# Kernel tuning notes

Hardware: AMD Instinct MI355X
Metric: run time of the kernel (lower is better)

The kernel has to match this reference:

```python
import jax, jax.numpy as jnp
import numpy as np

B, T = 128, 2048
O, E, L = 128, 512, 34  # o_size, embed_dim, num_letter


def setup_inputs() -> dict:
    key = jax.random.key(0)
    ks = jax.random.split(key, 16)
    u = lambda k, shape, s: jax.random.uniform(k, shape, jnp.float32, -s, s)
    hk = jax.random.normal(ks[0], (B, T, O), jnp.float32)
    hv = jax.random.normal(ks[1], (B, T, O), jnp.float32)
    y_1 = jax.random.normal(ks[2], (B, E), jnp.float32)
    c_1 = jax.random.normal(ks[3], (B, O), jnp.float32)
    sh_1 = jax.random.normal(ks[4], (B, O), jnp.float32)
    sc_1 = jax.random.normal(ks[5], (B, O), jnp.float32)
    # valid-length mask (each row has at least T//2 valid positions)
    lengths = jax.random.randint(ks[6], (B,), T // 2, T + 1)
    mask = (jnp.arange(T)[None, :] < lengths[:, None]).astype(jnp.float32)
    s_rnn = 1.0 / np.sqrt(O)
    W_ih = u(ks[7], (4 * O, O + E), s_rnn)
    b_ih = u(ks[8], (4 * O,), s_rnn)
    W_hh = u(ks[9], (4 * O, O), s_rnn)
    b_hh = u(ks[10], (4 * O,), s_rnn)
    s1 = 1.0 / np.sqrt(O)
    W1 = u(ks[11], (L, O), s1); b1 = u(ks[12], (L,), s1)
    W2 = u(ks[13], (L, O), s1); b2 = u(ks[14], (L,), s1)
    s3 = 1.0 / np.sqrt(L)
    W3 = u(ks[15], (L, L), s3); b3 = u(jax.random.fold_in(key, 99), (L,), s3)
    return {"hk": hk, "hv": hv, "y_1": y_1, "c_1": c_1, "sh_1": sh_1,
            "sc_1": sc_1, "mask": mask, "W_ih": W_ih, "b_ih": b_ih,
            "W_hh": W_hh, "b_hh": b_hh, "W1": W1, "b1": b1,
            "W2": W2, "b2": b2, "W3": W3, "b3": b3}


def reference(hk, hv, y_1, c_1, sh_1, sc_1, mask,
              W_ih, b_ih, W_hh, b_hh, W1, b1, W2, b2, W3, b3):
    # LSTMCell (PyTorch gate order: i, f, g, o)
    x = jnp.concatenate([y_1, c_1], axis=1)            # [B, O+E]
    gates = x @ W_ih.T + b_ih + sh_1 @ W_hh.T + b_hh   # [B, 4O]
    i, f, g, o = jnp.split(gates, 4, axis=1)
    sc = jax.nn.sigmoid(f) * sc_1 + jax.nn.sigmoid(i) * jnp.tanh(g)
    sh = jax.nn.sigmoid(o) * jnp.tanh(sc)
    # attention scores keyed on cell state sc (faithful to source)
    scores = jnp.einsum('bto,bo->bt', hk, sc)          # [B, T]
    attn = jax.nn.softmax(scores, axis=1) * mask
    attn = attn / jnp.sum(attn, axis=1, keepdims=True)
    c = jnp.einsum('bt,bto->bo', attn, hv)             # [B, O]
    out = jax.nn.relu(sh @ W1.T + b1 + c @ W2.T + b2)
    out = jax.nn.softmax(out @ W3.T + b3, axis=1)      # [B, L]
    return (out, c, sh, sc)
```

## Files before the change

kernel.cpp:

```cpp
#include <hip/hip_runtime.h>
#include <math.h>

#define BB 128
#define TT 2048
#define OO 128
#define EE 512
#define LL 34
#define XDIM 640
#define CHUNKS 16
#define CHUNK_LEN 128

__device__ __forceinline__ float sigmoidf_(float x) { return 1.0f / (1.0f + __expf(-x)); }

__global__ __launch_bounds__(256) void lstm_kernel(
    const float* __restrict__ y1, const float* __restrict__ c1,
    const float* __restrict__ sh1, const float* __restrict__ sc1,
    const float* __restrict__ Wih, const float* __restrict__ bih,
    const float* __restrict__ Whh, const float* __restrict__ bhh,
    float* __restrict__ out_sh, float* __restrict__ out_sc)
{
    __shared__ float xs[4][768];
    __shared__ float gbuf[4][4][16];
    const int tid = threadIdx.x;
    const int otile = blockIdx.x;
    const int qb = blockIdx.y * 4;

    for (int idx = tid; idx < 4 * 768; idx += 256) {
        int bi = idx / 768, k = idx - bi * 768;
        int b = qb + bi;
        float v;
        if (k < 512)      v = y1[b * EE + k];
        else if (k < 640) v = c1[b * OO + (k - 512)];
        else              v = sh1[b * OO + (k - 640)];
        xs[bi][k] = v;
    }
    __syncthreads();

    const int g = tid >> 6, l = tid & 63;
    #pragma unroll 2
    for (int i = 0; i < 16; ++i) {
        const int row = g * 128 + otile * 16 + i;
        const float* wr = Wih + (size_t)row * XDIM;
        float a0 = 0.f, a1 = 0.f, a2 = 0.f, a3 = 0.f;
        #pragma unroll
        for (int j = 0; j < 10; ++j) {
            float wv = wr[l + 64 * j];
            a0 += wv * xs[0][l + 64 * j];
            a1 += wv * xs[1][l + 64 * j];
            a2 += wv * xs[2][l + 64 * j];
            a3 += wv * xs[3][l + 64 * j];
        }
        const float* wh = Whh + (size_t)row * OO;
        #pragma unroll
        for (int j = 0; j < 2; ++j) {
            float wv = wh[l + 64 * j];
            a0 += wv * xs[0][640 + l + 64 * j];
            a1 += wv * xs[1][640 + l + 64 * j];
            a2 += wv * xs[2][640 + l + 64 * j];
            a3 += wv * xs[3][640 + l + 64 * j];
        }
        #pragma unroll
        for (int off = 32; off >= 1; off >>= 1) {
            a0 += __shfl_xor(a0, off);
            a1 += __shfl_xor(a1, off);
            a2 += __shfl_xor(a2, off);
            a3 += __shfl_xor(a3, off);
        }
        if (l == 0) {
            float bb = bih[row] + bhh[row];
            gbuf[g][0][i] = a0 + bb;
            gbuf[g][1][i] = a1 + bb;
            gbuf[g][2][i] = a2 + bb;
            gbuf[g][3][i] = a3 + bb;
        }
    }
    __syncthreads();

    if (tid < 64) {
        const int bi = tid >> 4, ol = tid & 15;
        const int b = qb + bi, o = otile * 16 + ol;
        float gi = gbuf[0][bi][ol], gf = gbuf[1][bi][ol];
        float gg = gbuf[2][bi][ol], go = gbuf[3][bi][ol];
        float sc = sigmoidf_(gf) * sc1[b * OO + o] + sigmoidf_(gi) * tanhf(gg);
        float sh = sigmoidf_(go) * tanhf(sc);
        out_sc[b * OO + o] = sc;
        out_sh[b * OO + o] = sh;
    }
}

__global__ __launch_bounds__(256) void scores_kernel(
    const float* __restrict__ hk, const float* __restrict__ mask,
    const float* __restrict__ sc, float* __restrict__ wbuf)
{
    const int b = blockIdx.y, chunk = blockIdx.x;
    const int tid = threadIdx.x;
    const int sg = tid >> 4, l = tid & 15;

    const float4 scA = *(const float4*)(sc + b * OO + l * 8);
    const float4 scB = *(const float4*)(sc + b * OO + l * 8 + 4);

    const int r0 = chunk * CHUNK_LEN + sg * 8;
    const float* mrow = mask + (size_t)b * TT + r0;
    const float* krow = hk + ((size_t)b * TT + r0) * OO;

    float s[8];
    #pragma unroll
    for (int i = 0; i < 8; ++i) {
        const bool valid = (mrow[i] != 0.f);
        float4 a = make_float4(0.f, 0.f, 0.f, 0.f);
        float4 c2 = make_float4(0.f, 0.f, 0.f, 0.f);
        if (valid) {
            a  = *(const float4*)(krow + (size_t)i * OO + l * 8);
            c2 = *(const float4*)(krow + (size_t)i * OO + l * 8 + 4);
        }
        s[i] = a.x * scA.x + a.y * scA.y + a.z * scA.z + a.w * scA.w
             + c2.x * scB.x + c2.y * scB.y + c2.z * scB.z + c2.w * scB.w;
    }
    #pragma unroll
    for (int i = 0; i < 8; ++i) {
        s[i] += __shfl_xor(s[i], 8);
        s[i] += __shfl_xor(s[i], 4);
        s[i] += __shfl_xor(s[i], 2);
        s[i] += __shfl_xor(s[i], 1);
    }
    float* wrow = wbuf + (size_t)b * TT + r0;
    #pragma unroll
    for (int i = 0; i < 8; ++i)
        if (l == i) wrow[i] = s[i];
}

__global__ __launch_bounds__(256) void softmax_kernel(
    float* __restrict__ wbuf, const float* __restrict__ mask)
{
    const int b = blockIdx.x, tid = threadIdx.x;
    const int lane = tid & 63, wv = tid >> 6;
    float* srow = wbuf + (size_t)b * TT;
    const float* mrow = mask + (size_t)b * TT;

    float sarr[8], earr[8];
    bool varr[8];
    float lm = -INFINITY;
    #pragma unroll
    for (int j = 0; j < 8; ++j) {
        int t = tid + 256 * j;
        sarr[j] = srow[t];
        varr[j] = (mrow[t] != 0.f);
        if (varr[j]) lm = fmaxf(lm, sarr[j]);
    }
    #pragma unroll
    for (int off = 32; off >= 1; off >>= 1) lm = fmaxf(lm, __shfl_xor(lm, off));
    __shared__ float red[4];
    if (lane == 0) red[wv] = lm;
    __syncthreads();
    const float M = fmaxf(fmaxf(red[0], red[1]), fmaxf(red[2], red[3]));

    float ls = 0.f;
    #pragma unroll
    for (int j = 0; j < 8; ++j) {
        earr[j] = varr[j] ? __expf(sarr[j] - M) : 0.f;
        ls += earr[j];
    }
    #pragma unroll
    for (int off = 32; off >= 1; off >>= 1) ls += __shfl_xor(ls, off);
    __syncthreads();
    if (lane == 0) red[wv] = ls;
    __syncthreads();
    const float inv = 1.f / (red[0] + red[1] + red[2] + red[3]);
    #pragma unroll
    for (int j = 0; j < 8; ++j) srow[tid + 256 * j] = earr[j] * inv;
}

__global__ __launch_bounds__(256) void wsum_kernel(
    const float* __restrict__ hv, const float* __restrict__ wbuf,
    float* __restrict__ ws_c)
{
    const int b = blockIdx.y, chunk = blockIdx.x;
    const int tid = threadIdx.x;
    __shared__ float wsh[CHUNK_LEN];
    __shared__ float pacc[8][128];

    if (tid < CHUNK_LEN)
        wsh[tid] = wbuf[(size_t)b * TT + chunk * CHUNK_LEN + tid];
    __syncthreads();

    const int o4 = tid & 31, rr = tid >> 5;
    const float* vbase = hv + ((size_t)b * TT + chunk * CHUNK_LEN) * OO + o4 * 4;
    float4 acc = make_float4(0.f, 0.f, 0.f, 0.f);
    #pragma unroll 8
    for (int j = 0; j < 16; ++j) {
        const int r = rr + 8 * j;
        const float wr = wsh[r];
        if (wr != 0.f) {
            float4 v = *(const float4*)(vbase + (size_t)r * OO);
            acc.x += wr * v.x;
            acc.y += wr * v.y;
            acc.z += wr * v.z;
            acc.w += wr * v.w;
        }
    }
    *(float4*)&pacc[rr][o4 * 4] = acc;
    __syncthreads();

    if (tid < 128) {
        float s = 0.f;
        #pragma unroll
        for (int i = 0; i < 8; ++i) s += pacc[i][tid];
        ws_c[((size_t)b * CHUNKS + chunk) * OO + tid] = s;
    }
}

__global__ __launch_bounds__(256) void final_kernel(
    const float* __restrict__ ws_c, const float* __restrict__ sh_in,
    const float* __restrict__ W1, const float* __restrict__ b1,
    const float* __restrict__ W2, const float* __restrict__ b2,
    const float* __restrict__ W3, const float* __restrict__ b3,
    float* __restrict__ out_p, float* __restrict__ out_c)
{
    const int b = blockIdx.x, tid = threadIdx.x;
    __shared__ float cbuf[128], shbuf[128], h1[LL], zz[LL], red2[2];

    if (tid < 128) {
        float s = 0.f;
        const float* base = ws_c + (size_t)b * CHUNKS * OO + tid;
        #pragma unroll
        for (int i = 0; i < CHUNKS; ++i) s += base[i * OO];
        cbuf[tid] = s;
        out_c[b * OO + tid] = s;
        shbuf[tid] = sh_in[b * OO + tid];
    }
    __syncthreads();

    const int o = tid >> 2, l2 = tid & 3;
    if (o < LL) {
        float a = 0.f;
        const float* w1r = W1 + o * OO;
        const float* w2r = W2 + o * OO;
        #pragma unroll 8
        for (int j = 0; j < 32; ++j) {
            int k = l2 + 4 * j;
            a += w1r[k] * shbuf[k] + w2r[k] * cbuf[k];
        }
        a += __shfl_xor(a, 1);
        a += __shfl_xor(a, 2);
        if (l2 == 0) h1[o] = fmaxf(a + b1[o] + b2[o], 0.f);
    }
    __syncthreads();

    if (o < LL) {
        float z = 0.f;
        const float* w3r = W3 + o * LL;
        for (int j = 0; j < 9; ++j) {
            int k = l2 + 4 * j;
            if (k < LL) z += w3r[k] * h1[k];
        }
        z += __shfl_xor(z, 1);
        z += __shfl_xor(z, 2);
        if (l2 == 0) zz[o] = z + b3[o];
    }
    __syncthreads();
    if (tid == 0) {
        float mm = zz[0];
        for (int i = 1; i < LL; i++) mm = fmaxf(mm, zz[i]);
        float ss = 0.f;
        for (int i = 0; i < LL; i++) ss += __expf(zz[i] - mm);
        red2[0] = mm; red2[1] = ss;
    }
    __syncthreads();
    if (tid < LL) out_p[b * LL + tid] = __expf(zz[tid] - red2[0]) / red2[1];
}

extern "C" void kernel_launch(void* const* d_in, const int* in_sizes, int n_in,
                              void* d_out, int out_size, void* d_ws, size_t ws_size,
                              hipStream_t stream) {
    (void)in_sizes; (void)n_in; (void)out_size; (void)ws_size;
    const float* hk   = (const float*)d_in[0];
    const float* hv   = (const float*)d_in[1];
    const float* y1   = (const float*)d_in[2];
    const float* c1   = (const float*)d_in[3];
    const float* sh1  = (const float*)d_in[4];
    const float* sc1  = (const float*)d_in[5];
    const float* mask = (const float*)d_in[6];
    const float* Wih  = (const float*)d_in[7];
    const float* bih  = (const float*)d_in[8];
    const float* Whh  = (const float*)d_in[9];
    const float* bhh  = (const float*)d_in[10];
    const float* W1   = (const float*)d_in[11];
    const float* b1   = (const float*)d_in[12];
    const float* W2   = (const float*)d_in[13];
    const float* b2   = (const float*)d_in[14];
    const float* W3   = (const float*)d_in[15];
    const float* b3   = (const float*)d_in[16];

    float* out    = (float*)d_out;
    float* out_c  = out + BB * LL;
    float* out_sh = out_c + BB * OO;
    float* out_sc = out_sh + BB * OO;

    float* wbuf = (float*)d_ws;
    float* ws_c = wbuf + (size_t)BB * TT;

    lstm_kernel<<<dim3(8, 32), 256, 0, stream>>>(y1, c1, sh1, sc1, Wih, bih, Whh, bhh,
                                                 out_sh, out_sc);
    scores_kernel<<<dim3(CHUNKS, BB), 256, 0, stream>>>(hk, mask, out_sc, wbuf);
    softmax_kernel<<<BB, 256, 0, stream>>>(wbuf, mask);
    wsum_kernel<<<dim3(CHUNKS, BB), 256, 0, stream>>>(hv, wbuf, ws_c);
    final_kernel<<<BB, 256, 0, stream>>>(ws_c, out_sh, W1, b1, W2, b2, W3, b3,
                                         out, out_c);
}
```

Before: 331.2 us.

## Fuse softmax into scores via per-chunk online max/sum, drop softmax kernel

Each scores block now computes a local max and exp-sum over its chunk, writes unnormalised exponentials plus a (max, sum) pair per chunk, and wsum rescales the chunk weights with the combined global max and sum. This removes the separate softmax kernel launch and its extra read/write pass over the score buffer. In exchange it adds a block-level reduction in scores and a small per-block combine in wsum, and it depends on the workspace being large enough to hold the new pbuf region.

```diff
diff --git a/kernel.cpp b/kernel.cpp
--- a/kernel.cpp
+++ b/kernel.cpp
@@ -90,7 +90,8 @@
 
 __global__ __launch_bounds__(256) void scores_kernel(
     const float* __restrict__ hk, const float* __restrict__ mask,
-    const float* __restrict__ sc, float* __restrict__ wbuf)
+    const float* __restrict__ sc, float* __restrict__ wbuf,
+    float2* __restrict__ pbuf)
 {
     const int b = blockIdx.y, chunk = blockIdx.x;
     const int tid = threadIdx.x;
@@ -104,12 +105,13 @@
     const float* krow = hk + ((size_t)b * TT + r0) * OO;
 
     float s[8];
+    bool val[8];
     #pragma unroll
     for (int i = 0; i < 8; ++i) {
-        const bool valid = (mrow[i] != 0.f);
+        val[i] = (mrow[i] != 0.f);
         float4 a = make_float4(0.f, 0.f, 0.f, 0.f);
         float4 c2 = make_float4(0.f, 0.f, 0.f, 0.f);
-        if (valid) {
+        if (val[i]) {
             a  = *(const float4*)(krow + (size_t)i * OO + l * 8);
             c2 = *(const float4*)(krow + (size_t)i * OO + l * 8 + 4);
         }
@@ -123,64 +125,64 @@
         s[i] += __shfl_xor(s[i], 2);
         s[i] += __shfl_xor(s[i], 1);
     }
+    float msg = -INFINITY;
+    #pragma unroll
+    for (int i = 0; i < 8; ++i) if (val[i]) msg = fmaxf(msg, s[i]);
+
+    __shared__ float sm[16], ssum[16];
+    if (l == 0) sm[sg] = msg;
+    __syncthreads();
+    float mc = sm[0];
+    #pragma unroll
+    for (int i = 1; i < 16; ++i) mc = fmaxf(mc, sm[i]);
+
+    float psum = 0.f;
+    float e[8];
+    #pragma unroll
+    for (int i = 0; i < 8; ++i) {
+        e[i] = val[i] ? __expf(s[i] - mc) : 0.f;
+        psum += e[i];
+    }
+    if (l == 0) ssum[sg] = psum;
     float* wrow = wbuf + (size_t)b * TT + r0;
     #pragma unroll
     for (int i = 0; i < 8; ++i)
-        if (l == i) wrow[i] = s[i];
-}
-
-__global__ __launch_bounds__(256) void softmax_kernel(
-    float* __restrict__ wbuf, const float* __restrict__ mask)
-{
-    const int b = blockIdx.x, tid = threadIdx.x;
-    const int lane = tid & 63, wv = tid >> 6;
-    float* srow = wbuf + (size_t)b * TT;
-    const float* mrow = mask + (size_t)b * TT;
-
-    float sarr[8], earr[8];
-    bool varr[8];
-    float lm = -INFINITY;
-    #pragma unroll
-    for (int j = 0; j < 8; ++j) {
-        int t = tid + 256 * j;
-        sarr[j] = srow[t];
-        varr[j] = (mrow[t] != 0.f);
-        if (varr[j]) lm = fmaxf(lm, sarr[j]);
-    }
-    #pragma unroll
-    for (int off = 32; off >= 1; off >>= 1) lm = fmaxf(lm, __shfl_xor(lm, off));
-    __shared__ float red[4];
-    if (lane == 0) red[wv] = lm;
-    __syncthreads();
-    const float M = fmaxf(fmaxf(red[0], red[1]), fmaxf(red[2], red[3]));
-
-    float ls = 0.f;
-    #pragma unroll
-    for (int j = 0; j < 8; ++j) {
-        earr[j] = varr[j] ? __expf(sarr[j] - M) : 0.f;
-        ls += earr[j];
-    }
-    #pragma unroll
-    for (int off = 32; off >= 1; off >>= 1) ls += __shfl_xor(ls, off);
-    __syncthreads();
-    if (lane == 0) red[wv] = ls;
-    __syncthreads();
-    const float inv = 1.f / (red[0] + red[1] + red[2] + red[3]);
-    #pragma unroll
-    for (int j = 0; j < 8; ++j) srow[tid + 256 * j] = earr[j] * inv;
+        if (l == i) wrow[i] = e[i];
+    __syncthreads();
+    if (tid == 0) {
+        float S = 0.f;
+        #pragma unroll
+        for (int i = 0; i < 16; ++i) S += ssum[i];
+        pbuf[(size_t)b * CHUNKS + chunk] = make_float2(mc, S);
+    }
 }
 
 __global__ __launch_bounds__(256) void wsum_kernel(
     const float* __restrict__ hv, const float* __restrict__ wbuf,
-    float* __restrict__ ws_c)
+    const float2* __restrict__ pbuf, float* __restrict__ ws_c)
 {
     const int b = blockIdx.y, chunk = blockIdx.x;
     const int tid = threadIdx.x;
+    __shared__ float marr[CHUNKS], Sarr[CHUNKS];
     __shared__ float wsh[CHUNK_LEN];
     __shared__ float pacc[8][128];
 
+    if (tid < CHUNKS) {
+        float2 p = pbuf[(size_t)b * CHUNKS + tid];
+        marr[tid] = p.x;
+        Sarr[tid] = p.y;
+    }
+    __syncthreads();
+    float M = marr[0];
+    #pragma unroll
+    for (int i = 1; i < CHUNKS; ++i) M = fmaxf(M, marr[i]);
+    float S = 0.f;
+    #pragma unroll
+    for (int i = 0; i < CHUNKS; ++i) S += Sarr[i] * __expf(marr[i] - M);
+    const float factor = __expf(marr[chunk] - M) / S;
+
     if (tid < CHUNK_LEN)
-        wsh[tid] = wbuf[(size_t)b * TT + chunk * CHUNK_LEN + tid];
+        wsh[tid] = wbuf[(size_t)b * TT + chunk * CHUNK_LEN + tid] * factor;
     __syncthreads();
 
     const int o4 = tid & 31, rr = tid >> 5;
@@ -296,14 +298,14 @@
     float* out_sh = out_c + BB * OO;
     float* out_sc = out_sh + BB * OO;
 
-    float* wbuf = (float*)d_ws;
-    float* ws_c = wbuf + (size_t)BB * TT;
+    float*  wbuf = (float*)d_ws;
+    float*  ws_c = wbuf + (size_t)BB * TT;
+    float2* pbuf = (float2*)(ws_c + (size_t)BB * CHUNKS * OO);
 
     lstm_kernel<<<dim3(8, 32), 256, 0, stream>>>(y1, c1, sh1, sc1, Wih, bih, Whh, bhh,
                                                  out_sh, out_sc);
-    scores_kernel<<<dim3(CHUNKS, BB), 256, 0, stream>>>(hk, mask, out_sc, wbuf);
-    softmax_kernel<<<BB, 256, 0, stream>>>(wbuf, mask);
-    wsum_kernel<<<dim3(CHUNKS, BB), 256, 0, stream>>>(hv, wbuf, ws_c);
+    scores_kernel<<<dim3(CHUNKS, BB), 256, 0, stream>>>(hk, mask, out_sc, wbuf, pbuf);
+    wsum_kernel<<<dim3(CHUNKS, BB), 256, 0, stream>>>(hv, wbuf, pbuf, ws_c);
     final_kernel<<<BB, 256, 0, stream>>>(ws_c, out_sh, W1, b1, W2, b2, W3, b3,
                                          out, out_c);
 }
```

Measured after the change: 328.2 us. About the same (-0.9%).

## Batch unconditional float4 loads in scores and weighted-sum kernels for memory parallelism

Applied to the files above, without the earlier changes.

Both streaming kernels are remapped so each half-wavefront reads a full 128-float row with contiguous float4 loads. Each thread issues eight independent loads before using any of them, which raises the number of memory requests in flight. The data-dependent skipping of masked or zero-weight rows is dropped, so every row of hk and hv is read. This trades extra bytes for regular, coalesced, branch-free loads. Correctness still relies on softmax applying the mask, and the cross-row reduction now uses an xor-32 shuffle plus a 4-way shared reduction.

```diff
diff --git a/kernel.cpp b/kernel.cpp
--- a/kernel.cpp
+++ b/kernel.cpp
@@ -89,44 +89,37 @@
 }
 
 __global__ __launch_bounds__(256) void scores_kernel(
-    const float* __restrict__ hk, const float* __restrict__ mask,
-    const float* __restrict__ sc, float* __restrict__ wbuf)
+    const float* __restrict__ hk, const float* __restrict__ sc,
+    float* __restrict__ wbuf)
 {
     const int b = blockIdx.y, chunk = blockIdx.x;
     const int tid = threadIdx.x;
-    const int sg = tid >> 4, l = tid & 15;
-
-    const float4 scA = *(const float4*)(sc + b * OO + l * 8);
-    const float4 scB = *(const float4*)(sc + b * OO + l * 8 + 4);
-
-    const int r0 = chunk * CHUNK_LEN + sg * 8;
-    const float* mrow = mask + (size_t)b * TT + r0;
-    const float* krow = hk + ((size_t)b * TT + r0) * OO;
-
-    float s[8];
-    #pragma unroll
-    for (int i = 0; i < 8; ++i) {
-        const bool valid = (mrow[i] != 0.f);
-        float4 a = make_float4(0.f, 0.f, 0.f, 0.f);
-        float4 c2 = make_float4(0.f, 0.f, 0.f, 0.f);
-        if (valid) {
-            a  = *(const float4*)(krow + (size_t)i * OO + l * 8);
-            c2 = *(const float4*)(krow + (size_t)i * OO + l * 8 + 4);
-        }
-        s[i] = a.x * scA.x + a.y * scA.y + a.z * scA.z + a.w * scA.w
-             + c2.x * scB.x + c2.y * scB.y + c2.z * scB.z + c2.w * scB.w;
-    }
-    #pragma unroll
-    for (int i = 0; i < 8; ++i) {
-        s[i] += __shfl_xor(s[i], 8);
-        s[i] += __shfl_xor(s[i], 4);
-        s[i] += __shfl_xor(s[i], 2);
-        s[i] += __shfl_xor(s[i], 1);
-    }
-    float* wrow = wbuf + (size_t)b * TT + r0;
-    #pragma unroll
-    for (int i = 0; i < 8; ++i)
-        if (l == i) wrow[i] = s[i];
+    const int w = tid >> 6, lane = tid & 63;
+    const int h = lane >> 5, l5 = lane & 31;
+
+    const float4 scv = *(const float4*)(sc + b * OO + l5 * 4);
+    const int rbase = chunk * CHUNK_LEN + w * 32;
+    const float* kbase = hk + ((size_t)b * TT + rbase) * OO + l5 * 4;
+    float* wrow = wbuf + (size_t)b * TT + rbase;
+
+    #pragma unroll
+    for (int batch = 0; batch < 2; ++batch) {
+        float4 kv[8];
+        #pragma unroll
+        for (int i = 0; i < 8; ++i)
+            kv[i] = *(const float4*)(kbase + (size_t)(batch * 16 + 2 * i + h) * OO);
+        #pragma unroll
+        for (int i = 0; i < 8; ++i) {
+            float p = kv[i].x * scv.x + kv[i].y * scv.y
+                    + kv[i].z * scv.z + kv[i].w * scv.w;
+            p += __shfl_xor(p, 1);
+            p += __shfl_xor(p, 2);
+            p += __shfl_xor(p, 4);
+            p += __shfl_xor(p, 8);
+            p += __shfl_xor(p, 16);
+            if (l5 == 0) wrow[batch * 16 + 2 * i + h] = p;
+        }
+    }
 }
 
 __global__ __launch_bounds__(256) void softmax_kernel(
@@ -176,35 +169,43 @@
 {
     const int b = blockIdx.y, chunk = blockIdx.x;
     const int tid = threadIdx.x;
-    __shared__ float wsh[CHUNK_LEN];
-    __shared__ float pacc[8][128];
-
-    if (tid < CHUNK_LEN)
-        wsh[tid] = wbuf[(size_t)b * TT + chunk * CHUNK_LEN + tid];
-    __syncthreads();
-
-    const int o4 = tid & 31, rr = tid >> 5;
-    const float* vbase = hv + ((size_t)b * TT + chunk * CHUNK_LEN) * OO + o4 * 4;
+    const int w = tid >> 6, lane = tid & 63;
+    const int h = lane >> 5, l5 = lane & 31;
+
+    const int rbase = chunk * CHUNK_LEN + w * 32;
+    const float* vbase = hv + ((size_t)b * TT + rbase) * OO + l5 * 4;
+    const float* wrow = wbuf + (size_t)b * TT + rbase;
+
     float4 acc = make_float4(0.f, 0.f, 0.f, 0.f);
-    #pragma unroll 8
-    for (int j = 0; j < 16; ++j) {
-        const int r = rr + 8 * j;
-        const float wr = wsh[r];
-        if (wr != 0.f) {
-            float4 v = *(const float4*)(vbase + (size_t)r * OO);
-            acc.x += wr * v.x;
-            acc.y += wr * v.y;
-            acc.z += wr * v.z;
-            acc.w += wr * v.w;
-        }
-    }
-    *(float4*)&pacc[rr][o4 * 4] = acc;
+    #pragma unroll
+    for (int batch = 0; batch < 2; ++batch) {
+        float4 vv[8];
+        float wr[8];
+        #pragma unroll
+        for (int i = 0; i < 8; ++i) {
+            const int r = batch * 16 + 2 * i + h;
+            vv[i] = *(const float4*)(vbase + (size_t)r * OO);
+            wr[i] = wrow[r];
+        }
+        #pragma unroll
+        for (int i = 0; i < 8; ++i) {
+            acc.x += wr[i] * vv[i].x;
+            acc.y += wr[i] * vv[i].y;
+            acc.z += wr[i] * vv[i].z;
+            acc.w += wr[i] * vv[i].w;
+        }
+    }
+    acc.x += __shfl_xor(acc.x, 32);
+    acc.y += __shfl_xor(acc.y, 32);
+    acc.z += __shfl_xor(acc.z, 32);
+    acc.w += __shfl_xor(acc.w, 32);
+
+    __shared__ float pacc[4][128];
+    if (h == 0) *(float4*)&pacc[w][l5 * 4] = acc;
     __syncthreads();
 
     if (tid < 128) {
-        float s = 0.f;
-        #pragma unroll
-        for (int i = 0; i < 8; ++i) s += pacc[i][tid];
+        float s = pacc[0][tid] + pacc[1][tid] + pacc[2][tid] + pacc[3][tid];
         ws_c[((size_t)b * CHUNKS + chunk) * OO + tid] = s;
     }
 }
@@ -301,7 +302,7 @@
 
     lstm_kernel<<<dim3(8, 32), 256, 0, stream>>>(y1, c1, sh1, sc1, Wih, bih, Whh, bhh,
                                                  out_sh, out_sc);
-    scores_kernel<<<dim3(CHUNKS, BB), 256, 0, stream>>>(hk, mask, out_sc, wbuf);
+    scores_kernel<<<dim3(CHUNKS, BB), 256, 0, stream>>>(hk, out_sc, wbuf);
     softmax_kernel<<<BB, 256, 0, stream>>>(wbuf, mask);
     wsum_kernel<<<dim3(CHUNKS, BB), 256, 0, stream>>>(hv, wbuf, ws_c);
     final_kernel<<<BB, 256, 0, stream>>>(ws_c, out_sh, W1, b1, W2, b2, W3, b3,
```

Result: no change. 337.5 us (+1.9%).
